# Kernel optimization log

Measured on AMD Instinct MI355X. Metric: run time of the kernel, lower is better.

Reference implementation:

```python
import jax, jax.numpy as jnp
import numpy as np

B, L, D, H, DFF, C = 16, 1024, 256, 4, 2048, 3
NS, NC = 4, 4
DH = D // H


def _ln(x, g, b):
    m = x.mean(-1, keepdims=True)
    v = ((x - m) ** 2).mean(-1, keepdims=True)
    return (x - m) / jnp.sqrt(v + 1e-5) * g + b


def setup_inputs() -> dict:
    key = jax.random.key(0)
    ks = jax.random.split(key, 24)
    n = lambda k, s: jax.random.normal(k, s, jnp.float32) * 0.02
    return {
        'shape_idxs': jax.random.randint(ks[0], (B, L), 0, NS, jnp.int32),
        'color_idxs': jax.random.randint(ks[1], (B, L), 0, NC, jnp.int32),
        'shape_emb': n(ks[2], (NS, D)),
        'color_emb': n(ks[3], (NC, D)),
        'Wq': n(ks[4], (D, D)), 'bq': jnp.zeros((D,)),
        'Wk': n(ks[5], (D, D)), 'bk': jnp.zeros((D,)),
        'Wv': n(ks[6], (D, D)), 'bv': jnp.zeros((D,)),
        'Wo': n(ks[7], (D, D)), 'bo': jnp.zeros((D,)),
        'g1': jnp.ones((D,)), 'be1': jnp.zeros((D,)),
        'W1': n(ks[8], (D, DFF)), 'bf1': jnp.zeros((DFF,)),
        'W2': n(ks[9], (DFF, D)), 'bf2': jnp.zeros((D,)),
        'g2': jnp.ones((D,)), 'be2': jnp.zeros((D,)),
        'Wl': n(ks[10], (D, C)), 'bl': jnp.zeros((C,)),
        'Wp1': n(ks[11], (D, D)), 'bp1': jnp.zeros((D,)),
        'Wp2': n(ks[12], (D, 1)), 'bp2': jnp.zeros((1,)),
        'wc': n(ks[13], (1, 1)), 'bc': jnp.zeros((1,)),
    }


def reference(shape_idxs, color_idxs, shape_emb, color_emb, Wq, bq, Wk, bk, Wv, bv,
              Wo, bo, g1, be1, W1, bf1, W2, bf2, g2, be2, Wl, bl,
              Wp1, bp1, Wp2, bp2, wc, bc):
    # embed (dropout is identity in eval)
    x = shape_emb[shape_idxs] + color_emb[color_idxs]  # [B,L,D]
    # post-norm transformer encoder layer (PyTorch default)
    heads = lambda t: t.reshape(B, L, H, DH)
    q, k, v = heads(x @ Wq + bq), heads(x @ Wk + bk), heads(x @ Wv + bv)
    scores = jnp.einsum('blhd,bmhd->bhlm', q, k) / jnp.sqrt(jnp.float32(DH))
    attn = jax.nn.softmax(scores, axis=-1)
    ctx = jnp.einsum('bhlm,bmhd->blhd', attn, v).reshape(B, L, D)
    y = _ln(x + ctx @ Wo + bo, g1, be1)
    ff = jax.nn.relu(y @ W1 + bf1) @ W2 + bf2
    y = _ln(y + ff, g2, be2)  # trans_out [B,L,D]
    # latent logits / KL(prior || probs) with batchmean reduction
    logits = y @ Wl + bl
    logp = jax.nn.log_softmax(logits, axis=-1)
    prior = 1.0 / C
    kl_loss = jnp.sum(prior * (jnp.log(jnp.float32(prior)) - logp)) / B
    # data-dependent boundary segmentation (argmax of probs == argmax of logits)
    boundaries = (jnp.argmax(logits, axis=-1) == 0)
    boundaries = boundaries.at[:, 0].set(True)
    closed = boundaries & (jnp.arange(L) > 0)  # closure at l>0 ends segment at l
    seg_id = jnp.cumsum(closed.astype(jnp.int32), axis=1) - closed  # exclusive cumsum
    gid = (jnp.arange(B)[:, None] * L + seg_id).reshape(-1)  # global segment ids
    sums = jax.ops.segment_sum(y.reshape(B * L, D), gid, num_segments=B * L)
    counts = jax.ops.segment_sum(jnp.ones((B * L,), jnp.float32), gid, num_segments=B * L)
    means = sums / jnp.maximum(counts, 1.0)[:, None]  # per-segment mean [B*L,D]
    # predicate net + composition, mean over valid segments
    preds = jax.nn.sigmoid(jax.nn.relu(means @ Wp1 + bp1) @ Wp2 + bp2)  # [B*L,1]
    comp = (preds * wc[0, 0] + bc[0]).reshape(B, L)
    valid = (counts > 0).reshape(B, L).astype(jnp.float32)
    mean_comp = jnp.sum(comp * valid, axis=1) / jnp.sum(valid, axis=1)
    final_scores = jax.nn.sigmoid(mean_comp)
    return final_scores, kl_loss
```

## Files before the change

### kernel.cpp

```cpp
#include <hip/hip_runtime.h>


typedef unsigned short u16;
typedef u16    u16x4  __attribute__((ext_vector_type(4)));
typedef u16    u16x8  __attribute__((ext_vector_type(8)));
typedef __bf16 bf16x8 __attribute__((ext_vector_type(8)));
typedef float  f32x4  __attribute__((ext_vector_type(4)));

__device__ __forceinline__ float bf2f(u16 u) {
    union { unsigned int i; float f; } v; v.i = ((unsigned int)u) << 16; return v.f;
}
__device__ __forceinline__ u16 f2bf(float f) {
    union { float f; unsigned int i; } v; v.f = f;
    unsigned int r = (v.i + 0x7FFFu + ((v.i >> 16) & 1u)) >> 16;
    return (u16)r;
}
__device__ __forceinline__ u16 f2bf_fast(float f) {
    union { __bf16 h; u16 u; } v; v.h = (__bf16)f; return v.u;
}
__device__ __forceinline__ void gll16(const u16* g, u16* l) {
    __builtin_amdgcn_global_load_lds((__attribute__((address_space(1))) void*)(u16*)g,
                                     (__attribute__((address_space(3))) void*)l, 16, 0, 0);
}
__device__ __forceinline__ int get_mode(const int* __restrict__ detp) {
    int s = 0;
#pragma unroll 8
    for (int i = 0; i < 64; ++i) s += detp[i];
    return s > 16;
}

__global__ __launch_bounds__(256) void k_detect(const u16* __restrict__ w1raw,
                                                int* __restrict__ detp) {
    int i = blockIdx.x * 256 + threadIdx.x;
    int bad = 0;
    for (int k = i; k < 65536; k += 64 * 256) {
        unsigned v = w1raw[k] & 0x7FFFu;
        if (v >= 0x7F80u) bad++;
    }
    for (int off = 32; off >= 1; off >>= 1) bad += __shfl_xor(bad, off);
    __shared__ int bs[4];
    if ((threadIdx.x & 63) == 0) bs[threadIdx.x >> 6] = bad;
    __syncthreads();
    if (threadIdx.x == 0) detp[blockIdx.x] = bs[0] + bs[1] + bs[2] + bs[3];
}
__global__ void k_sentinel_f32(float* __restrict__ out, int code) {
    int t = threadIdx.x;
    if (t < 17) out[t] = (float)code;
}

struct PrepTab {
    const void* src[7];
    u16*        dst[7];
    int         K[7], N[7];
    float       scale[7];
    int         tstart[8];
    const void* isrc[17];
    unsigned    idstoff[17];
    int         in[17];
    float       iscale[17];
    u16*        ing;
};
__global__ __launch_bounds__(256) void k_prep(PrepTab tt, const int* __restrict__ detp) {
    int m = get_mode(detp);
    int bx = blockIdx.x;
    if (bx >= tt.tstart[7]) {
        int t = bx - tt.tstart[7];
        int n = tt.in[t];
        float sc = tt.iscale[t];
        u16* dst = tt.ing + tt.idstoff[t];
        for (int i = threadIdx.x; i < n; i += 256) {
            float v = m ? ((const float*)tt.isrc[t])[i] : bf2f(((const u16*)tt.isrc[t])[i]);
            dst[i] = f2bf(v * sc);
        }
        return;
    }
    __shared__ u16 tile[32][33];
    int wgt = 0;
#pragma unroll
    for (int i = 1; i < 7; ++i) if (bx >= tt.tstart[i]) wgt = i;
    int local = bx - tt.tstart[wgt];
    int K = tt.K[wgt], N = tt.N[wgt];
    float sc = tt.scale[wgt];
    int ntx = N >> 5;
    int txt = local % ntx, tyt = local / ntx;
    const void* W = tt.src[wgt];
    u16* Wt = tt.dst[wgt];
    int tx = threadIdx.x & 31, ty = threadIdx.x >> 5;
    int n = txt * 32 + tx;
    for (int i = ty; i < 32; i += 8) {
        size_t idx = (size_t)(tyt * 32 + i) * N + n;
        float v = m ? ((const float*)W)[idx] : bf2f(((const u16*)W)[idx]);
        tile[i][tx] = f2bf(v * sc);
    }
    __syncthreads();
    int k2 = tyt * 32 + tx;
    for (int i = ty; i < 32; i += 8) {
        int n2 = txt * 32 + i;
        Wt[(size_t)n2 * K + k2] = tile[tx][i];
    }
}

__global__ __launch_bounds__(256) void k_embed(const int* __restrict__ si,
                                               const int* __restrict__ ci,
                                               const void* __restrict__ se,
                                               const void* __restrict__ ce,
                                               u16* __restrict__ X,
                                               const int* __restrict__ detp) {
    int m = get_mode(detp);
    int t = blockIdx.x * 256 + threadIdx.x;
    int row = t >> 5, seg = (t & 31) * 8;
    int s = si[row], c = ci[row];
    u16x8 o;
    if (m) {
        const float* sp = (const float*)se + s * 256 + seg;
        const float* cp = (const float*)ce + c * 256 + seg;
#pragma unroll
        for (int e = 0; e < 8; ++e) o[e] = f2bf(sp[e] + cp[e]);
    } else {
        u16x8 a = *(const u16x8*)((const u16*)se + s * 256 + seg);
        u16x8 b = *(const u16x8*)((const u16*)ce + c * 256 + seg);
#pragma unroll
        for (int e = 0; e < 8; ++e) o[e] = f2bf(bf2f(a[e]) + bf2f(b[e]));
    }
    *(u16x8*)&X[(size_t)row * 256 + seg] = o;
}

__global__ __launch_bounds__(256) void k_gemm_bt(const u16* __restrict__ A,
                                                 const u16* __restrict__ Bt,
                                                 const u16* __restrict__ bias,
                                                 u16* __restrict__ C,
                                                 int N, int K, int relu, int gx) {
    __shared__ u16 As[128][32];
    __shared__ u16 Bs[128][32];
    const int tid = threadIdx.x;
    const int xcd = blockIdx.x & 7, j = blockIdx.x >> 3;
    const int m0 = (xcd * 16 + j / gx) * 128, n0 = (j % gx) * 128;
    const int lane = tid & 63, wid = tid >> 6;
    const int wm = (wid & 1) * 64, wn = (wid >> 1) * 64;
    const int m16 = lane & 15, quad = lane >> 4;
    f32x4 acc[4][4] = {};
    const int arow = tid >> 2;
    const int ac8  = (tid & 3) * 8;
    const u16* Ap0 = A  + (size_t)(m0 + arow) * K + ac8;
    const u16* Ap1 = A  + (size_t)(m0 + 64 + arow) * K + ac8;
    const u16* Bp0 = Bt + (size_t)(n0 + arow) * K + ac8;
    const u16* Bp1 = Bt + (size_t)(n0 + 64 + arow) * K + ac8;
    u16* lA0 = &As[arow][ac8];
    u16* lA1 = &As[64 + arow][ac8];
    u16* lB0 = &Bs[arow][ac8];
    u16* lB1 = &Bs[64 + arow][ac8];

    for (int k0 = 0; k0 < K; k0 += 32) {
        __syncthreads();
        gll16(Ap0 + k0, lA0);
        gll16(Ap1 + k0, lA1);
        gll16(Bp0 + k0, lB0);
        gll16(Bp1 + k0, lB1);
        __syncthreads();
        bf16x8 af[4], bfv[4];
#pragma unroll
        for (int i = 0; i < 4; ++i)
            af[i] = *(const bf16x8*)&As[wm + i * 16 + m16][quad * 8];
#pragma unroll
        for (int j2 = 0; j2 < 4; ++j2)
            bfv[j2] = *(const bf16x8*)&Bs[wn + j2 * 16 + m16][quad * 8];
#pragma unroll
        for (int i = 0; i < 4; ++i)
#pragma unroll
            for (int j2 = 0; j2 < 4; ++j2)
                acc[i][j2] = __builtin_amdgcn_mfma_f32_16x16x32_bf16(
                    af[i], bfv[j2], acc[i][j2], 0, 0, 0);
    }

#pragma unroll
    for (int i = 0; i < 4; ++i) {
        int row = m0 + wm + i * 16 + quad * 4;
#pragma unroll
        for (int j2 = 0; j2 < 4; ++j2) {
            int col = n0 + wn + j2 * 16 + m16;
            float bv = bf2f(bias[col]);
#pragma unroll
            for (int r = 0; r < 4; ++r) {
                float v = acc[i][j2][r] + bv;
                if (relu) v = fmaxf(v, 0.f);
                C[(size_t)(row + r) * N + col] = f2bf_fast(v);
            }
        }
    }
}

__global__ __launch_bounds__(256) void k_gemm64(const u16* __restrict__ A,
                                                const u16* __restrict__ Bt,
                                                const u16* __restrict__ bias,
                                                u16* __restrict__ C,
                                                int N, int K, int relu,
                                                int gx, int mtpx,
                                                u16* __restrict__ vt) {
    __shared__ u16 As0[64][32], As1[64][32];
    __shared__ u16 Bs0[128][32], Bs1[128][32];
    const int tid = threadIdx.x;
    const int xcd = blockIdx.x & 7, j = blockIdx.x >> 3;
    const int m0 = (xcd * mtpx + j / gx) * 64, n0 = (j % gx) * 128;
    const int vmode = (vt != nullptr) && (n0 >= 512);
    const int lane = tid & 63, wid = tid >> 6;
    const int wm = (wid & 1) * 32, wn = (wid >> 1) * 64;
    const int m16 = lane & 15, quad = lane >> 4;
    f32x4 acc[2][4] = {};
    const int arow = tid >> 2;
    const int ac8  = (tid & 3) * 8;
    const u16* Ap  = A  + (size_t)(m0 + arow) * K + ac8;
    const u16* Bp0 = Bt + (size_t)(n0 + arow) * K + ac8;
    const u16* Bp1 = Bt + (size_t)(n0 + 64 + arow) * K + ac8;
    u16* lA0  = &As0[arow][ac8];
    u16* lA1  = &As1[arow][ac8];
    u16* lB00 = &Bs0[arow][ac8];
    u16* lB01 = &Bs0[64 + arow][ac8];
    u16* lB10 = &Bs1[arow][ac8];
    u16* lB11 = &Bs1[64 + arow][ac8];

    for (int k0 = 0; k0 < K; k0 += 64) {
        __syncthreads();
        gll16(Ap + k0,        lA0);
        gll16(Ap + k0 + 32,   lA1);
        gll16(Bp0 + k0,       lB00);
        gll16(Bp0 + k0 + 32,  lB10);
        gll16(Bp1 + k0,       lB01);
        gll16(Bp1 + k0 + 32,  lB11);
        __syncthreads();
#pragma unroll
        for (int ks = 0; ks < 2; ++ks) {
            bf16x8 af[2], bfv[4];
#pragma unroll
            for (int i = 0; i < 2; ++i)
                af[i] = ks == 0 ? *(const bf16x8*)&As0[wm + i * 16 + m16][quad * 8]
                                : *(const bf16x8*)&As1[wm + i * 16 + m16][quad * 8];
#pragma unroll
            for (int j2 = 0; j2 < 4; ++j2)
                bfv[j2] = ks == 0 ? *(const bf16x8*)&Bs0[wn + j2 * 16 + m16][quad * 8]
                                  : *(const bf16x8*)&Bs1[wn + j2 * 16 + m16][quad * 8];
#pragma unroll
            for (int i = 0; i < 2; ++i)
#pragma unroll
                for (int j2 = 0; j2 < 4; ++j2)
                    acc[i][j2] = __builtin_amdgcn_mfma_f32_16x16x32_bf16(
                        af[i], bfv[j2], acc[i][j2], 0, 0, 0);
        }
    }

#pragma unroll
    for (int i = 0; i < 2; ++i) {
        int row = m0 + wm + i * 16 + quad * 4;
#pragma unroll
        for (int j2 = 0; j2 < 4; ++j2) {
            int col = n0 + wn + j2 * 16 + m16;
            float bv = bf2f(bias[col]);
            if (vmode) {
                int ch = col - 512;
                u16x4 o;
#pragma unroll
                for (int r = 0; r < 4; ++r) o[r] = f2bf_fast(acc[i][j2][r] + bv);
                size_t vb = ((size_t)((row >> 10) * 4 + (ch >> 6)) * 64 + (ch & 63)) * 1024
                          + (row & 1023);
                *(u16x4*)&vt[vb] = o;
            } else {
#pragma unroll
                for (int r = 0; r < 4; ++r) {
                    float v = acc[i][j2][r] + bv;
                    if (relu) v = fmaxf(v, 0.f);
                    C[(size_t)(row + r) * N + col] = f2bf_fast(v);
                }
            }
        }
    }
}

__global__ __launch_bounds__(256) void k_gemm64n(const u16* __restrict__ A,
                                                 const u16* __restrict__ Bt,
                                                 const u16* __restrict__ bias,
                                                 u16* __restrict__ C,
                                                 int N, int K, int relu,
                                                 int gnx, int mtpx,
                                                 const float* __restrict__ gate) {
    __shared__ u16 As0[64][32], As1[64][32];
    __shared__ u16 Bs0[64][32], Bs1[64][32];
    const int tid = threadIdx.x;
    const int xcd = blockIdx.x & 7, j = blockIdx.x >> 3;
    const int m0 = (xcd * mtpx + j / gnx) * 64, n0 = (j % gnx) * 64;
    if (gate && gate[m0] == 0.f) return;
    const int lane = tid & 63, w = tid >> 6;
    const int m16 = lane & 15, quad = lane >> 4;
    f32x4 acc[4] = {};
    const int arow = tid >> 2;
    const int ac8  = (tid & 3) * 8;
    const u16* Ap = A  + (size_t)(m0 + arow) * K + ac8;
    const u16* Bp = Bt + (size_t)(n0 + arow) * K + ac8;
    u16* lA0 = &As0[arow][ac8];
    u16* lA1 = &As1[arow][ac8];
    u16* lB0 = &Bs0[arow][ac8];
    u16* lB1 = &Bs1[arow][ac8];

    for (int k0 = 0; k0 < K; k0 += 64) {
        __syncthreads();
        gll16(Ap + k0,       lA0);
        gll16(Ap + k0 + 32,  lA1);
        gll16(Bp + k0,       lB0);
        gll16(Bp + k0 + 32,  lB1);
        __syncthreads();
#pragma unroll
        for (int ks = 0; ks < 2; ++ks) {
            bf16x8 af = ks == 0 ? *(const bf16x8*)&As0[w * 16 + m16][quad * 8]
                                : *(const bf16x8*)&As1[w * 16 + m16][quad * 8];
#pragma unroll
            for (int nt = 0; nt < 4; ++nt) {
                bf16x8 bfv = ks == 0 ? *(const bf16x8*)&Bs0[nt * 16 + m16][quad * 8]
                                     : *(const bf16x8*)&Bs1[nt * 16 + m16][quad * 8];
                acc[nt] = __builtin_amdgcn_mfma_f32_16x16x32_bf16(af, bfv, acc[nt], 0, 0, 0);
            }
        }
    }

#pragma unroll
    for (int nt = 0; nt < 4; ++nt) {
        int col = n0 + nt * 16 + m16;
        float bv = bf2f(bias[col]);
        int row = m0 + w * 16 + quad * 4;
#pragma unroll
        for (int r = 0; r < 4; ++r) {
            float v = acc[nt][r] + bv;
            if (relu) v = fmaxf(v, 0.f);
            C[(size_t)(row + r) * N + col] = f2bf_fast(v);
        }
    }
}

__global__ __launch_bounds__(256) void k_attn_mfma(const u16* __restrict__ QKV,
                                                   const u16* __restrict__ VT,
                                                   u16* __restrict__ CTX) {
    __shared__ u16 Ks[64][72];
    __shared__ u16 Vts[64][72];
    __shared__ u16 Ps[4][16][72];
    const int tid = threadIdx.x, lane = tid & 63, w = tid >> 6;
    const int quad = lane >> 4, c = lane & 15;
    const int blk = blockIdx.x;
    const int xcd = blk & 7, local = blk >> 3;
    const int bh = xcd * 8 + (local >> 4);
    const int qt = local & 15;
    const int b = bh >> 2, h = bh & 3;
    const int qrow0 = b * 1024 + qt * 64;

    const u16* qptr = QKV + (size_t)(qrow0 + w * 16 + c) * 768 + h * 64;
    bf16x8 aq0 = *(const bf16x8*)(qptr + quad * 8);
    bf16x8 aq1 = *(const bf16x8*)(qptr + 32 + quad * 8);

    bf16x8 ones;
    {
        union { u16 u; __bf16 h; } v; v.u = 0x3F80;
#pragma unroll
        for (int e = 0; e < 8; ++e) ones[e] = v.h;
    }

    f32x4 acc_o[4] = {};
    f32x4 acc_l = {};

    const u16* kbase  = QKV + (size_t)(b * 1024) * 768 + 256 + h * 64;
    const u16* vtbase = VT + (size_t)(bh * 64) * 1024;
    const int skk = tid >> 3, sc8 = (tid & 7) * 8;

    for (int t = 0; t < 16; ++t) {
        __syncthreads();
#pragma unroll
        for (int it = 0; it < 2; ++it) {
            int rr = skk + 32 * it;
            *(u16x8*)&Ks[rr][sc8]  = *(const u16x8*)(kbase + (size_t)(t * 64 + rr) * 768 + sc8);
            *(u16x8*)&Vts[rr][sc8] = *(const u16x8*)(vtbase + (size_t)rr * 1024 + t * 64 + sc8);
        }
        __syncthreads();

        f32x4 s[4];
#pragma unroll
        for (int nt = 0; nt < 4; ++nt) {
            f32x4 z = {};
            bf16x8 bk0 = *(const bf16x8*)&Ks[nt * 16 + c][quad * 8];
            bf16x8 bk1 = *(const bf16x8*)&Ks[nt * 16 + c][32 + quad * 8];
            z = __builtin_amdgcn_mfma_f32_16x16x32_bf16(aq0, bk0, z, 0, 0, 0);
            s[nt] = __builtin_amdgcn_mfma_f32_16x16x32_bf16(aq1, bk1, z, 0, 0, 0);
        }

#pragma unroll
        for (int nt = 0; nt < 4; ++nt)
#pragma unroll
            for (int r = 0; r < 4; ++r)
                Ps[w][quad * 4 + r][nt * 16 + c] = f2bf_fast(exp2f(fminf(s[nt][r], 80.f)));

#pragma unroll
        for (int ks = 0; ks < 2; ++ks) {
            bf16x8 ap = *(const bf16x8*)&Ps[w][c][ks * 32 + quad * 8];
            acc_l = __builtin_amdgcn_mfma_f32_16x16x32_bf16(ap, ones, acc_l, 0, 0, 0);
#pragma unroll
            for (int nt = 0; nt < 4; ++nt) {
                bf16x8 bv = *(const bf16x8*)&Vts[nt * 16 + c][ks * 32 + quad * 8];
                acc_o[nt] = __builtin_amdgcn_mfma_f32_16x16x32_bf16(ap, bv, acc_o[nt], 0, 0, 0);
            }
        }
    }

#pragma unroll
    for (int nt = 0; nt < 4; ++nt) {
        int col = h * 64 + nt * 16 + c;
#pragma unroll
        for (int r = 0; r < 4; ++r) {
            int row = qrow0 + w * 16 + quad * 4 + r;
            CTX[(size_t)row * 256 + col] = f2bf_fast(acc_o[nt][r] / acc_l[r]);
        }
    }
}

__global__ __launch_bounds__(256) void k_ln(const u16* __restrict__ A,
                                            const u16* __restrict__ R,
                                            const u16* __restrict__ g,
                                            const u16* __restrict__ be,
                                            u16* __restrict__ out) {
    int w = threadIdx.x >> 6, lane = threadIdx.x & 63;
    int row = blockIdx.x * 4 + w;
    size_t base = (size_t)row * 256 + lane * 4;
    u16x4 a4 = *(const u16x4*)&A[base];
    u16x4 r4 = *(const u16x4*)&R[base];
    float v[4];
    float s = 0.f, sq = 0.f;
#pragma unroll
    for (int j = 0; j < 4; ++j) {
        v[j] = bf2f(a4[j]) + bf2f(r4[j]);
        s += v[j]; sq += v[j] * v[j];
    }
    for (int off = 32; off >= 1; off >>= 1) { s += __shfl_xor(s, off); sq += __shfl_xor(sq, off); }
    float mean = s * (1.f / 256.f);
    float var  = sq * (1.f / 256.f) - mean * mean;
    float rs   = rsqrtf(var + 1e-5f);
    u16x4 o;
#pragma unroll
    for (int j = 0; j < 4; ++j) {
        int d = lane * 4 + j;
        o[j] = f2bf((v[j] - mean) * rs * bf2f(g[d]) + bf2f(be[d]));
    }
    *(u16x4*)&out[base] = o;
}

__global__ __launch_bounds__(256) void k_logits(const u16* __restrict__ FFO,
                                                const u16* __restrict__ Y1,
                                                const u16* __restrict__ g2,
                                                const u16* __restrict__ be2,
                                                const u16* __restrict__ Wl,
                                                const u16* __restrict__ bl,
                                                u16* __restrict__ Y2,
                                                float* __restrict__ klpart,
                                                int* __restrict__ flags) {
    const int tid = threadIdx.x, lane = tid & 63, w = tid >> 6;
    float wv[4][3], gv[4], bev[4];
#pragma unroll
    for (int j = 0; j < 4; ++j) {
        int d = lane * 4 + j;
        gv[j]  = bf2f(g2[d]);
        bev[j] = bf2f(be2[d]);
#pragma unroll
        for (int c = 0; c < 3; ++c) wv[j][c] = bf2f(Wl[d * 3 + c]);
    }
    const float b0 = bf2f(bl[0]), b1 = bf2f(bl[1]), b2 = bf2f(bl[2]);
    float klsum = 0.f;
    const int row0 = blockIdx.x * 16 + w * 4;
    for (int i = 0; i < 4; ++i) {
        int row = row0 + i;
        size_t base = (size_t)row * 256 + lane * 4;
        u16x4 f4 = *(const u16x4*)&FFO[base];
        u16x4 y4 = *(const u16x4*)&Y1[base];
        float v[4];
        float s = 0.f, sq = 0.f;
#pragma unroll
        for (int j = 0; j < 4; ++j) {
            v[j] = bf2f(f4[j]) + bf2f(y4[j]);
            s += v[j]; sq += v[j] * v[j];
        }
        for (int off = 32; off >= 1; off >>= 1) { s += __shfl_xor(s, off); sq += __shfl_xor(sq, off); }
        float mean = s * (1.f / 256.f);
        float var  = sq * (1.f / 256.f) - mean * mean;
        float rs   = rsqrtf(var + 1e-5f);
        u16x4 o;
        float a0 = 0.f, a1 = 0.f, a2 = 0.f;
#pragma unroll
        for (int j = 0; j < 4; ++j) {
            float yn = (v[j] - mean) * rs * gv[j] + bev[j];
            o[j] = f2bf(yn);
            float y = bf2f(o[j]);
            a0 += y * wv[j][0]; a1 += y * wv[j][1]; a2 += y * wv[j][2];
        }
        *(u16x4*)&Y2[base] = o;
        for (int off = 32; off >= 1; off >>= 1) {
            a0 += __shfl_xor(a0, off); a1 += __shfl_xor(a1, off); a2 += __shfl_xor(a2, off);
        }
        if (lane == 0) {
            float l0 = a0 + b0, l1 = a1 + b1, l2 = a2 + b2;
            float mx = fmaxf(l0, fmaxf(l1, l2));
            float lse = mx + __logf(__expf(l0 - mx) + __expf(l1 - mx) + __expf(l2 - mx));
            klsum += lse - (l0 + l1 + l2) * (1.f / 3.f) - 1.0986122886681098f;
            int am = 0; float bv = l0;
            if (l1 > bv) { bv = l1; am = 1; }
            if (l2 > bv) { am = 2; }
            int l = row & 1023;
            flags[row] = (am == 0 && l != 0) ? 1 : 0;
        }
    }
    __shared__ float kls[4];
    if (lane == 0) kls[w] = klsum;
    __syncthreads();
    if (tid == 0) klpart[blockIdx.x] = kls[0] + kls[1] + kls[2] + kls[3];
}

__global__ void k_scan(const int* __restrict__ flags, int* __restrict__ seg) {
    __shared__ int wsum[16];
    int b = blockIdx.x, t = threadIdx.x;
    int lane = t & 63, w = t >> 6;
    int f = flags[b * 1024 + t];
    int x = f;
#pragma unroll
    for (int off = 1; off < 64; off <<= 1) {
        int v = __shfl_up(x, off);
        if (lane >= off) x += v;
    }
    if (lane == 63) wsum[w] = x;
    __syncthreads();
    if (w == 0) {
        int s = (lane < 16) ? wsum[lane] : 0;
#pragma unroll
        for (int off = 1; off < 16; off <<= 1) {
            int v = __shfl_up(s, off);
            if (lane >= off) s += v;
        }
        if (lane < 16) wsum[lane] = s;
    }
    __syncthreads();
    int prefix = (w > 0) ? wsum[w - 1] : 0;
    seg[b * 1024 + t] = prefix + x - f;
}

__global__ __launch_bounds__(64) void k_segmean(const u16* __restrict__ Y,
                                                const int* __restrict__ seg,
                                                u16* __restrict__ means,
                                                float* __restrict__ cnt) {
    int g = blockIdx.x, lane = threadIdx.x;
    int b = g >> 10, s = g & 1023;
    const int* sb = seg + b * 1024;
    int target = s + (lane & 1);
    int lo = 0, hi = 1024;
    while (lo < hi) {
        int mid = (lo + hi) >> 1;
        if (sb[mid] < target) lo = mid + 1; else hi = mid;
    }
    int start = __shfl(lo, 0);
    int end   = __shfl(lo, 1);
    int n = end - start;
    if (lane == 0) cnt[g] = (float)n;
    if (n <= 0) return;
    f32x4 acc = {};
    for (int row = start; row < end; ++row) {
        u16x4 y4 = *(const u16x4*)&Y[(size_t)(b * 1024 + row) * 256 + lane * 4];
        acc[0] += bf2f(y4[0]); acc[1] += bf2f(y4[1]);
        acc[2] += bf2f(y4[2]); acc[3] += bf2f(y4[3]);
    }
    float inv = 1.f / (float)n;
    u16x4 o;
#pragma unroll
    for (int j = 0; j < 4; ++j) o[j] = f2bf(acc[j] * inv);
    *(u16x4*)&means[(size_t)g * 256 + lane * 4] = o;
}

__global__ __launch_bounds__(256) void k_preds(const u16* __restrict__ T,
                                               const u16* __restrict__ Wp2,
                                               const u16* __restrict__ bp2,
                                               const u16* __restrict__ wc,
                                               const u16* __restrict__ bc,
                                               const float* __restrict__ cnt,
                                               float* __restrict__ predp) {
    const int tid = threadIdx.x, lane = tid & 63, w = tid >> 6;
    float lwp[4];
#pragma unroll
    for (int j = 0; j < 4; ++j) lwp[j] = bf2f(Wp2[lane * 4 + j]);
    const float fb = bf2f(bp2[0]), fw = bf2f(wc[0]), fc = bf2f(bc[0]);
    float csum = 0.f, vsum = 0.f;
    const int g0 = blockIdx.x * 16 + w * 4;
    if (cnt[g0] != 0.f) {
        for (int i = 0; i < 4; ++i) {
            int g = g0 + i;
            u16x4 t4 = *(const u16x4*)&T[(size_t)g * 256 + lane * 4];
            float a = 0.f;
#pragma unroll
            for (int j = 0; j < 4; ++j) a += bf2f(t4[j]) * lwp[j];
            for (int off = 32; off >= 1; off >>= 1) a += __shfl_xor(a, off);
            if (lane == 0 && cnt[g] > 0.f) {
                float pred = 1.f / (1.f + __expf(-(a + fb)));
                csum += pred * fw + fc;
                vsum += 1.f;
            }
        }
    }
    __shared__ float cs[4], vs[4];
    if (lane == 0) { cs[w] = csum; vs[w] = vsum; }
    __syncthreads();
    if (tid == 0) {
        predp[2 * blockIdx.x]     = cs[0] + cs[1] + cs[2] + cs[3];
        predp[2 * blockIdx.x + 1] = vs[0] + vs[1] + vs[2] + vs[3];
    }
}

__global__ void k_final(const float* __restrict__ predp, const float* __restrict__ klp,
                        const int* __restrict__ detp, void* __restrict__ outv) {
    int t = threadIdx.x;
    float k = 0.f;
    for (int i = t; i < 1024; i += 64) k += klp[i];
    for (int off = 32; off >= 1; off >>= 1) k += __shfl_xor(k, off);
    float ktot = __shfl(k, 0);
    int batch = t >> 2, ch = t & 3;
    float c = 0.f, v = 0.f;
    for (int i = 0; i < 16; ++i) {
        int blk = batch * 64 + ch * 16 + i;
        c += predp[2 * blk];
        v += predp[2 * blk + 1];
    }
    c += __shfl_xor(c, 1); c += __shfl_xor(c, 2);
    v += __shfl_xor(v, 1); v += __shfl_xor(v, 2);
    int mode = get_mode(detp);
    if ((t & 3) == 0) {
        float d = v, nm = c;
        if (!(d > 0.f)) d = 1.f;
        if (isnan(nm) || isinf(nm)) nm = 0.f;
        float val = 1.f / (1.f + __expf(-nm / d));
        if (mode) ((float*)outv)[batch] = val;
        else      ((u16*)outv)[batch]   = f2bf(val);
    }
    if (t == 1) {
        float val = ktot * (1.f / 16.f);
        if (isnan(val) || isinf(val)) val = 0.f;
        if (mode) ((float*)outv)[16] = val;
        else      ((u16*)outv)[16]   = f2bf(val);
    }
}

extern "C" void kernel_launch(void* const* d_in, const int* in_sizes, int n_in,
                              void* d_out, int out_size, void* d_ws, size_t ws_size,
                              hipStream_t stream) {
    const int* shape_idxs = (const int*)d_in[0];
    const int* color_idxs = (const int*)d_in[1];
    char* ws = (char*)d_ws;
    const size_t MB = 1024 * 1024;

    if (ws_size < 90 * MB) {
        int wsMB = (int)(ws_size >> 20); if (wsMB > 250) wsMB = 250;
        k_sentinel_f32<<<1, 32, 0, stream>>>((float*)d_out, 200 + wsMB);
        return;
    }

    u16*   X     = (u16*)(ws);
    u16*   QKVb  = (u16*)(ws + 8 * MB);
    u16*   VT    = (u16*)(ws + 32 * MB);
    u16*   CTX   = (u16*)(ws + 40 * MB);
    u16*   CTXP  = (u16*)(ws + 48 * MB);
    u16*   Y1    = (u16*)(ws + 64 * MB);
    u16*   Hb    = (u16*)(ws);
    u16*   FFO   = (u16*)(ws + 72 * MB);
    u16*   Y2    = (u16*)(ws);
    u16*   MEANS = (u16*)(ws + 24 * MB);
    u16*   TB    = (u16*)(ws + 32 * MB);
    int*   FLAGS = (int*)(ws + 80 * MB);
    int*   SEG   = (int*)(ws + 80 * MB + 65536);
    float* CNT   = (float*)(ws + 80 * MB + 131072);
    float* KLP   = (float*)(ws + 80 * MB + 262144);
    float* PREDP = (float*)(ws + 80 * MB + 327680);
    u16*   W3T   = (u16*)(ws + 81 * MB);
    u16*   WoT   = (u16*)(ws + 81 * MB + 786432);
    u16*   Wp1T  = (u16*)(ws + 81 * MB + 917504);
    u16*   W1T   = (u16*)(ws + 82 * MB);
    u16*   W2T   = (u16*)(ws + 83 * MB);
    int*   DETP  = (int*)(ws + 84 * MB);
    u16*   ING   = (u16*)(ws + 85 * MB);

    const float QSCALE = 0.125f * 1.44269504f;

    PrepTab tt;
    const void* tsrc[7] = {d_in[4], d_in[6], d_in[8], d_in[10], d_in[22], d_in[14], d_in[16]};
    u16* tdst[7] = {W3T, W3T + 256 * 256, W3T + 512 * 256, WoT, Wp1T, W1T, W2T};
    int tK[7] = {256, 256, 256, 256, 256, 256, 2048};
    int tN[7] = {256, 256, 256, 256, 256, 2048, 256};
    int ts = 0;
    for (int i = 0; i < 7; ++i) {
        tt.src[i] = tsrc[i]; tt.dst[i] = tdst[i]; tt.K[i] = tK[i]; tt.N[i] = tN[i];
        tt.scale[i] = (i == 0) ? QSCALE : 1.0f;
        tt.tstart[i] = ts;
        ts += (tK[i] >> 5) * (tN[i] >> 5);
    }
    tt.tstart[7] = ts;

    static const int II[17]  = {5, 7, 9, 11, 12, 13, 15, 17, 18, 19, 20, 21, 23, 24, 25, 26, 27};
    static const int IN[17]  = {256, 256, 256, 256, 256, 256, 2048, 256, 256, 256, 768, 3, 256, 256, 1, 1, 1};
    unsigned off = 0;
    for (int i = 0; i < 17; ++i) {
        tt.isrc[i] = d_in[II[i]];
        tt.in[i] = IN[i];
        tt.iscale[i] = 1.0f;
        if (i == 0) { tt.idstoff[0] = off; off += 768; }
        else if (i == 1) tt.idstoff[1] = tt.idstoff[0] + 256;
        else if (i == 2) tt.idstoff[2] = tt.idstoff[0] + 512;
        else { tt.idstoff[i] = off; off += (unsigned)((IN[i] + 8) & ~7); }
    }
    tt.iscale[0] = QSCALE;
    tt.ing = ING;
    const u16* ib3  = ING + tt.idstoff[0];
    const u16* ibo  = ING + tt.idstoff[3];
    const u16* ig1  = ING + tt.idstoff[4];  const u16* ibe1 = ING + tt.idstoff[5];
    const u16* ibf1 = ING + tt.idstoff[6];  const u16* ibf2 = ING + tt.idstoff[7];
    const u16* ig2  = ING + tt.idstoff[8];  const u16* ibe2 = ING + tt.idstoff[9];
    const u16* iWl  = ING + tt.idstoff[10]; const u16* ibl  = ING + tt.idstoff[11];
    const u16* ibp1 = ING + tt.idstoff[12]; const u16* iWp2 = ING + tt.idstoff[13];
    const u16* ibp2 = ING + tt.idstoff[14]; const u16* iwc  = ING + tt.idstoff[15];
    const u16* ibc  = ING + tt.idstoff[16];

    k_detect<<<64, 256, 0, stream>>>((const u16*)d_in[14], DETP);
    k_prep<<<ts + 17, 256, 0, stream>>>(tt, DETP);
    k_embed<<<2048, 256, 0, stream>>>(shape_idxs, color_idxs, d_in[2], d_in[3], X, DETP);
    k_gemm64<<<1536, 256, 0, stream>>>(X, W3T, ib3, QKVb, 768, 256, 0, 6, 32, VT);
    k_attn_mfma<<<1024, 256, 0, stream>>>(QKVb, VT, CTX);
    k_gemm64n<<<1024, 256, 0, stream>>>(CTX, WoT, ibo, CTXP, 256, 256, 0, 4, 32, nullptr);
    k_ln<<<4096, 256, 0, stream>>>(CTXP, X, ig1, ibe1, Y1);
    k_gemm_bt<<<16 * 128, 256, 0, stream>>>(Y1, W1T, ibf1, Hb, 2048, 256, 1, 16);
    k_gemm64n<<<1024, 256, 0, stream>>>(Hb, W2T, ibf2, FFO, 256, 2048, 0, 4, 32, nullptr);
    k_logits<<<1024, 256, 0, stream>>>(FFO, Y1, ig2, ibe2, iWl, ibl, Y2, KLP, FLAGS);
    k_scan<<<16, 1024, 0, stream>>>(FLAGS, SEG);
    k_segmean<<<16384, 64, 0, stream>>>(Y2, SEG, MEANS, CNT);
    k_gemm64n<<<1024, 256, 0, stream>>>(MEANS, Wp1T, ibp1, TB, 256, 256, 1, 4, 32, CNT);
    k_preds<<<1024, 256, 0, stream>>>(TB, iWp2, ibp2, iwc, ibc, CNT, PREDP);
    k_final<<<1, 64, 0, stream>>>(PREDP, KLP, DETP, d_out);
}
```

Baseline: 299.3 us.

## Fold dtype detection and embedding into prep kernel; widen gemm64n K-step

The separate detection kernel is removed. Each prep block and the final kernel now detect the input dtype locally by scanning the first 16K entries of W1. The embedding kernel is merged into the prep launch as extra blocks, so two launches go away. The 64-wide N GEMM now loads four 32-wide K slices per barrier pair instead of two, halving its synchronisation count but doubling its LDS use. The cost is that every prep block rereads 32KB of W1 for detection, which adds redundant L2 traffic, and the detection threshold now looks at a smaller sample.

After: 388.5 us. 29.8% more time.

```diff
diff --git a/kernel.cpp b/kernel.cpp
--- a/kernel.cpp
+++ b/kernel.cpp
@@ -22,27 +22,25 @@
     __builtin_amdgcn_global_load_lds((__attribute__((address_space(1))) void*)(u16*)g,
                                      (__attribute__((address_space(3))) void*)l, 16, 0, 0);
 }
-__device__ __forceinline__ int get_mode(const int* __restrict__ detp) {
-    int s = 0;
-#pragma unroll 8
-    for (int i = 0; i < 64; ++i) s += detp[i];
-    return s > 16;
-}
-
-__global__ __launch_bounds__(256) void k_detect(const u16* __restrict__ w1raw,
-                                                int* __restrict__ detp) {
-    int i = blockIdx.x * 256 + threadIdx.x;
+__device__ __forceinline__ int detect_mode_block(const u16* __restrict__ w1raw) {
+    __shared__ int bs[4];
+    __shared__ int ms;
+    int tid = threadIdx.x, nt = blockDim.x;
+    if (tid < 4) bs[tid] = 0;
+    __syncthreads();
     int bad = 0;
-    for (int k = i; k < 65536; k += 64 * 256) {
+    for (int k = tid; k < 16384; k += nt) {
         unsigned v = w1raw[k] & 0x7FFFu;
         if (v >= 0x7F80u) bad++;
     }
     for (int off = 32; off >= 1; off >>= 1) bad += __shfl_xor(bad, off);
-    __shared__ int bs[4];
-    if ((threadIdx.x & 63) == 0) bs[threadIdx.x >> 6] = bad;
+    if ((tid & 63) == 0) bs[tid >> 6] = bad;
     __syncthreads();
-    if (threadIdx.x == 0) detp[blockIdx.x] = bs[0] + bs[1] + bs[2] + bs[3];
-}
+    if (tid == 0) ms = (bs[0] + bs[1] + bs[2] + bs[3]) > 8;
+    __syncthreads();
+    return ms;
+}
+
 __global__ void k_sentinel_f32(float* __restrict__ out, int code) {
     int t = threadIdx.x;
     if (t < 17) out[t] = (float)code;
@@ -59,12 +57,39 @@
     int         in[17];
     float       iscale[17];
     u16*        ing;
+    const int*  si;
+    const int*  ci;
+    const void* se;
+    const void* ce;
+    u16*        X;
+    const u16*  w1raw;
 };
-__global__ __launch_bounds__(256) void k_prep(PrepTab tt, const int* __restrict__ detp) {
-    int m = get_mode(detp);
+__global__ __launch_bounds__(256) void k_prep(PrepTab tt) {
+    int m = detect_mode_block(tt.w1raw);
     int bx = blockIdx.x;
-    if (bx >= tt.tstart[7]) {
-        int t = bx - tt.tstart[7];
+    int ibase = tt.tstart[7];
+    if (bx >= ibase + 17) {
+        int eb = bx - (ibase + 17);
+        int t = eb * 256 + threadIdx.x;
+        int row = t >> 5, seg = (t & 31) * 8;
+        int s = tt.si[row], c = tt.ci[row];
+        u16x8 o;
+        if (m) {
+            const float* sp = (const float*)tt.se + s * 256 + seg;
+            const float* cp = (const float*)tt.ce + c * 256 + seg;
+#pragma unroll
+            for (int e = 0; e < 8; ++e) o[e] = f2bf(sp[e] + cp[e]);
+        } else {
+            u16x8 a = *(const u16x8*)((const u16*)tt.se + s * 256 + seg);
+            u16x8 b = *(const u16x8*)((const u16*)tt.ce + c * 256 + seg);
+#pragma unroll
+            for (int e = 0; e < 8; ++e) o[e] = f2bf(bf2f(a[e]) + bf2f(b[e]));
+        }
+        *(u16x8*)&tt.X[(size_t)row * 256 + seg] = o;
+        return;
+    }
+    if (bx >= ibase) {
+        int t = bx - ibase;
         int n = tt.in[t];
         float sc = tt.iscale[t];
         u16* dst = tt.ing + tt.idstoff[t];
@@ -98,31 +123,6 @@
         int n2 = txt * 32 + i;
         Wt[(size_t)n2 * K + k2] = tile[tx][i];
     }
-}
-
-__global__ __launch_bounds__(256) void k_embed(const int* __restrict__ si,
-                                               const int* __restrict__ ci,
-                                               const void* __restrict__ se,
-                                               const void* __restrict__ ce,
-                                               u16* __restrict__ X,
-                                               const int* __restrict__ detp) {
-    int m = get_mode(detp);
-    int t = blockIdx.x * 256 + threadIdx.x;
-    int row = t >> 5, seg = (t & 31) * 8;
-    int s = si[row], c = ci[row];
-    u16x8 o;
-    if (m) {
-        const float* sp = (const float*)se + s * 256 + seg;
-        const float* cp = (const float*)ce + c * 256 + seg;
-#pragma unroll
-        for (int e = 0; e < 8; ++e) o[e] = f2bf(sp[e] + cp[e]);
-    } else {
-        u16x8 a = *(const u16x8*)((const u16*)se + s * 256 + seg);
-        u16x8 b = *(const u16x8*)((const u16*)ce + c * 256 + seg);
-#pragma unroll
-        for (int e = 0; e < 8; ++e) o[e] = f2bf(bf2f(a[e]) + bf2f(b[e]));
-    }
-    *(u16x8*)&X[(size_t)row * 256 + seg] = o;
 }
 
 __global__ __launch_bounds__(256) void k_gemm_bt(const u16* __restrict__ A,
@@ -281,8 +281,8 @@
                                                  int N, int K, int relu,
                                                  int gnx, int mtpx,
                                                  const float* __restrict__ gate) {
-    __shared__ u16 As0[64][32], As1[64][32];
-    __shared__ u16 Bs0[64][32], Bs1[64][32];
+    __shared__ u16 As[4][64][32];
+    __shared__ u16 Bs[4][64][32];
     const int tid = threadIdx.x;
     const int xcd = blockIdx.x & 7, j = blockIdx.x >> 3;
     const int m0 = (xcd * mtpx + j / gnx) * 64, n0 = (j % gnx) * 64;
@@ -294,26 +294,24 @@
     const int ac8  = (tid & 3) * 8;
     const u16* Ap = A  + (size_t)(m0 + arow) * K + ac8;
     const u16* Bp = Bt + (size_t)(n0 + arow) * K + ac8;
-    u16* lA0 = &As0[arow][ac8];
-    u16* lA1 = &As1[arow][ac8];
-    u16* lB0 = &Bs0[arow][ac8];
-    u16* lB1 = &Bs1[arow][ac8];
-
-    for (int k0 = 0; k0 < K; k0 += 64) {
+    u16* lA[4]; u16* lB[4];
+#pragma unroll
+    for (int q = 0; q < 4; ++q) { lA[q] = &As[q][arow][ac8]; lB[q] = &Bs[q][arow][ac8]; }
+
+    for (int k0 = 0; k0 < K; k0 += 128) {
         __syncthreads();
-        gll16(Ap + k0,       lA0);
-        gll16(Ap + k0 + 32,  lA1);
-        gll16(Bp + k0,       lB0);
-        gll16(Bp + k0 + 32,  lB1);
+#pragma unroll
+        for (int q = 0; q < 4; ++q) {
+            gll16(Ap + k0 + q * 32, lA[q]);
+            gll16(Bp + k0 + q * 32, lB[q]);
+        }
         __syncthreads();
 #pragma unroll
-        for (int ks = 0; ks < 2; ++ks) {
-            bf16x8 af = ks == 0 ? *(const bf16x8*)&As0[w * 16 + m16][quad * 8]
-                                : *(const bf16x8*)&As1[w * 16 + m16][quad * 8];
+        for (int ks = 0; ks < 4; ++ks) {
+            bf16x8 af = *(const bf16x8*)&As[ks][w * 16 + m16][quad * 8];
 #pragma unroll
             for (int nt = 0; nt < 4; ++nt) {
-                bf16x8 bfv = ks == 0 ? *(const bf16x8*)&Bs0[nt * 16 + m16][quad * 8]
-                                     : *(const bf16x8*)&Bs1[nt * 16 + m16][quad * 8];
+                bf16x8 bfv = *(const bf16x8*)&Bs[ks][nt * 16 + m16][quad * 8];
                 acc[nt] = __builtin_amdgcn_mfma_f32_16x16x32_bf16(af, bfv, acc[nt], 0, 0, 0);
             }
         }
@@ -611,7 +609,8 @@
 }
 
 __global__ void k_final(const float* __restrict__ predp, const float* __restrict__ klp,
-                        const int* __restrict__ detp, void* __restrict__ outv) {
+                        const u16* __restrict__ w1raw, void* __restrict__ outv) {
+    int mode = detect_mode_block(w1raw);
     int t = threadIdx.x;
     float k = 0.f;
     for (int i = t; i < 1024; i += 64) k += klp[i];
@@ -626,7 +625,6 @@
     }
     c += __shfl_xor(c, 1); c += __shfl_xor(c, 2);
     v += __shfl_xor(v, 1); v += __shfl_xor(v, 2);
-    int mode = get_mode(detp);
     if ((t & 3) == 0) {
         float d = v, nm = c;
         if (!(d > 0.f)) d = 1.f;
@@ -678,10 +676,10 @@
     u16*   Wp1T  = (u16*)(ws + 81 * MB + 917504);
     u16*   W1T   = (u16*)(ws + 82 * MB);
     u16*   W2T   = (u16*)(ws + 83 * MB);
-    int*   DETP  = (int*)(ws + 84 * MB);
     u16*   ING   = (u16*)(ws + 85 * MB);
 
     const float QSCALE = 0.125f * 1.44269504f;
+    const u16* w1raw = (const u16*)d_in[14];
 
     PrepTab tt;
     const void* tsrc[7] = {d_in[4], d_in[6], d_in[8], d_in[10], d_in[22], d_in[14], d_in[16]};
@@ -711,6 +709,9 @@
     }
     tt.iscale[0] = QSCALE;
     tt.ing = ING;
+    tt.si = shape_idxs; tt.ci = color_idxs;
+    tt.se = d_in[2]; tt.ce = d_in[3];
+    tt.X = X; tt.w1raw = w1raw;
     const u16* ib3  = ING + tt.idstoff[0];
     const u16* ibo  = ING + tt.idstoff[3];
     const u16* ig1  = ING + tt.idstoff[4];  const u16* ibe1 = ING + tt.idstoff[5];
@@ -721,9 +722,7 @@
     const u16* ibp2 = ING + tt.idstoff[14]; const u16* iwc  = ING + tt.idstoff[15];
     const u16* ibc  = ING + tt.idstoff[16];
 
-    k_detect<<<64, 256, 0, stream>>>((const u16*)d_in[14], DETP);
-    k_prep<<<ts + 17, 256, 0, stream>>>(tt, DETP);
-    k_embed<<<2048, 256, 0, stream>>>(shape_idxs, color_idxs, d_in[2], d_in[3], X, DETP);
+    k_prep<<<ts + 17 + 2048, 256, 0, stream>>>(tt);
     k_gemm64<<<1536, 256, 0, stream>>>(X, W3T, ib3, QKVb, 768, 256, 0, 6, 32, VT);
     k_attn_mfma<<<1024, 256, 0, stream>>>(QKVb, VT, CTX);
     k_gemm64n<<<1024, 256, 0, stream>>>(CTX, WoT, ibo, CTXP, 256, 256, 0, 4, 32, nullptr);
@@ -735,5 +734,5 @@
     k_segmean<<<16384, 64, 0, stream>>>(Y2, SEG, MEANS, CNT);
     k_gemm64n<<<1024, 256, 0, stream>>>(MEANS, Wp1T, ibp1, TB, 256, 256, 1, 4, 32, CNT);
     k_preds<<<1024, 256, 0, stream>>>(TB, iWp2, ibp2, iwc, ibc, CNT, PREDP);
-    k_final<<<1, 64, 0, stream>>>(PREDP, KLP, DETP, d_out);
-}
+    k_final<<<1, 64, 0, stream>>>(PREDP, KLP, w1raw, d_out);
+}
```
